# Optimization experiments

Measured on AMD Instinct MI355X. Metric: run time of the kernel, lower is better.

## Reference

```python
import jax, jax.numpy as jnp
import numpy as np

N_NODES = 100000
N_EDGES = 1600000
IN_CH, HID_CH, OUT_CH = 64, 128, 128


def setup_inputs() -> dict:
    key = jax.random.key(0)
    ks = jax.random.split(key, 10)
    x = jax.random.normal(ks[0], (N_NODES, IN_CH), dtype=jnp.float32)
    edge_index = jax.random.randint(ks[1], (2, N_EDGES), 0, N_NODES, dtype=jnp.int64 if jax.config.jax_enable_x64 else jnp.int32)
    edge_weight = jax.random.uniform(ks[2], (N_EDGES,), dtype=jnp.float32)
    def glorot(k, fan_in, fan_out):
        lim = np.sqrt(6.0 / (fan_in + fan_out)).astype(np.float32)
        return jax.random.uniform(k, (fan_in, fan_out), minval=-lim, maxval=lim, dtype=jnp.float32)
    W1 = glorot(ks[3], IN_CH, HID_CH)
    b1 = jnp.zeros((HID_CH,), jnp.float32)
    W2 = glorot(ks[4], HID_CH, HID_CH)
    b2 = jnp.zeros((HID_CH,), jnp.float32)
    W3 = glorot(ks[5], HID_CH, OUT_CH)
    b3 = jnp.zeros((OUT_CH,), jnp.float32)
    return {"x": x, "edge_index": edge_index, "edge_weight": edge_weight,
            "W1": W1, "b1": b1, "W2": W2, "b2": b2, "W3": W3, "b3": b3}


def _gcn_norm(edge_index, edge_weight, num_nodes):
    # add self-loops with weight 1 (PyG GCNConv default)
    loop = jnp.arange(num_nodes, dtype=edge_index.dtype)
    src = jnp.concatenate([edge_index[0], loop])
    dst = jnp.concatenate([edge_index[1], loop])
    w = jnp.concatenate([edge_weight, jnp.ones((num_nodes,), edge_weight.dtype)])
    deg = jax.ops.segment_sum(w, dst, num_segments=num_nodes)
    dinv = jnp.where(deg > 0, jax.lax.rsqrt(deg), 0.0)
    norm = dinv[src] * w * dinv[dst]
    return src, dst, norm


def _gcn_layer(x, W, b, src, dst, norm, num_nodes):
    h = x @ W                                  # [N, C_out]
    msg = h[src] * norm[:, None]               # gather + scale, [E+N, C_out]
    agg = jax.ops.segment_sum(msg, dst, num_segments=num_nodes)
    return agg + b


def reference(x, edge_index, edge_weight, W1, b1, W2, b2, W3, b3):
    n = x.shape[0]
    src, dst, norm = _gcn_norm(edge_index, edge_weight, n)
    h = jax.nn.silu(_gcn_layer(x, W1, b1, src, dst, norm, n))
    h = jax.nn.silu(_gcn_layer(h, W2, b2, src, dst, norm, n))
    h = jax.nn.silu(_gcn_layer(h, W3, b3, src, dst, norm, n))
    # single-graph global mean pool (batch == zeros)
    return jnp.mean(h, axis=0, keepdims=True)  # [1, out_channels]
```

## Files before the change

### kernel.cpp

```cpp
#include <hip/hip_runtime.h>

#define C 128
#define INCH 64
#define FIXP 33554432.0f

typedef unsigned short bf16_t;
typedef float f32x4 __attribute__((ext_vector_type(4)));
typedef unsigned int u32x4 __attribute__((ext_vector_type(4)));

__device__ __forceinline__ float silu_f(float v) {
    return v / (1.0f + __expf(-v));
}

__device__ __forceinline__ bf16_t f2bf(float f) {
    unsigned b = __float_as_uint(f);
    return (bf16_t)((b + 0x7FFFu + ((b >> 16) & 1u)) >> 16);
}
__device__ __forceinline__ float bf2f(unsigned u) {
    return __uint_as_float(u << 16);
}

__device__ __forceinline__ void mfma16x16x32(f32x4& d, u32x4 a, u32x4 b) {
    asm("v_mfma_f32_16x16x32_bf16 %0, %1, %2, %0" : "+v"(d) : "v"(a), "v"(b));
}


template<int NCH> struct VecN;
template<> struct VecN<4> { using T = float4; };
template<> struct VecN<2> { using T = float2; };

template<int NCH> struct LdB;
template<> struct LdB<4> {
    static __device__ __forceinline__ float4 ld(const bf16_t* p) {
        ushort4 u = *(const ushort4*)p;
        return make_float4(bf2f(u.x), bf2f(u.y), bf2f(u.z), bf2f(u.w));
    }
};
template<> struct LdB<2> {
    static __device__ __forceinline__ float2 ld(const bf16_t* p) {
        ushort2 u = *(const ushort2*)p;
        return make_float2(bf2f(u.x), bf2f(u.y));
    }
};

template<int NCH> struct StB;
template<> struct StB<4> {
    static __device__ __forceinline__ void st(bf16_t* p, float4 v) {
        *(ushort4*)p = make_ushort4(f2bf(v.x), f2bf(v.y), f2bf(v.z), f2bf(v.w));
    }
};
template<> struct StB<2> {
    static __device__ __forceinline__ void st(bf16_t* p, float2 v) {
        *(ushort2*)p = make_ushort2(f2bf(v.x), f2bf(v.y));
    }
};

__device__ __forceinline__ float4 vfma(const float4 v, float n, float4 a) {
    a.x = fmaf(v.x, n, a.x); a.y = fmaf(v.y, n, a.y);
    a.z = fmaf(v.z, n, a.z); a.w = fmaf(v.w, n, a.w); return a;
}
__device__ __forceinline__ float2 vfma(const float2 v, float n, float2 a) {
    a.x = fmaf(v.x, n, a.x); a.y = fmaf(v.y, n, a.y); return a;
}
__device__ __forceinline__ float4 vmul(const float4 v, float s) {
    return make_float4(v.x * s, v.y * s, v.z * s, v.w * s);
}
__device__ __forceinline__ float2 vmul(const float2 v, float s) {
    return make_float2(v.x * s, v.y * s);
}
__device__ __forceinline__ float4 vadd(const float4 a, const float4 b) {
    return make_float4(a.x + b.x, a.y + b.y, a.z + b.z, a.w + b.w);
}
__device__ __forceinline__ float2 vadd(const float2 a, const float2 b) {
    return make_float2(a.x + b.x, a.y + b.y);
}


__global__ void init_k(unsigned long long* packed, int n) {
    int i = blockIdx.x * blockDim.x + threadIdx.x;
    if (i < n) packed[i] = 0ull;
}

__global__ void hist_k(const int* __restrict__ dst, const float* __restrict__ w,
                       unsigned long long* packed, int* __restrict__ rank, int E) {
    int e = blockIdx.x * blockDim.x + threadIdx.x;
    if (e < E) {
        unsigned fx = (unsigned)(w[e] * FIXP + 0.5f);
        unsigned long long old =
            atomicAdd(&packed[dst[e]], (1ull << 32) | (unsigned long long)fx);
        rank[e] = (int)(old >> 32);
    }
}

__global__ void extract_k(const unsigned long long* __restrict__ packed,
                          int* counts, float* dinv, int n) {
    int i = blockIdx.x * blockDim.x + threadIdx.x;
    if (i < n) {
        unsigned long long p = packed[i];
        counts[i] = (int)(p >> 32);
        float deg = 1.0f + (float)(unsigned)(p & 0xffffffffull) * (1.0f / FIXP);
        dinv[i] = rsqrtf(deg);
    }
}


__global__ void cvt_bf16_k(const float* __restrict__ in, bf16_t* __restrict__ out, int n4) {
    int i = blockIdx.x * blockDim.x + threadIdx.x;
    if (i < n4) {
        float4 v = *(const float4*)&in[(size_t)i * 4];
        ushort4 u = make_ushort4(f2bf(v.x), f2bf(v.y), f2bf(v.z), f2bf(v.w));
        *(ushort4*)&out[(size_t)i * 4] = u;
    }
}


__global__ void wfrag_k(const float* __restrict__ W, bf16_t* __restrict__ Wf, int K) {
    int idx = blockIdx.x * blockDim.x + threadIdx.x;
    if (idx >= K * 128) return;
    int KS = K / 32;
    int j = idx & 7;
    int lane = (idx >> 3) & 63;
    int rest = idx >> 9;
    int ks = rest % KS;
    int nt = rest / KS;
    int col = nt * 16 + (lane & 15);
    int k = ks * 32 + (lane >> 4) * 8 + j;
    Wf[idx] = f2bf(W[k * 128 + col]);
}


#define SCAN_T 256
#define SCAN_E 1024

__global__ void scan1_k(const int* __restrict__ counts, int* rowptr, int* bsums, int N) {
    __shared__ int s[SCAN_T];
    int t = threadIdx.x;
    int base = blockIdx.x * SCAN_E + t * 4;
    int v[4];
    #pragma unroll
    for (int j = 0; j < 4; ++j) { int i = base + j; v[j] = (i < N) ? counts[i] : 0; }
    int sum = v[0] + v[1] + v[2] + v[3];
    s[t] = sum; __syncthreads();
    for (int off = 1; off < SCAN_T; off <<= 1) {
        int y = (t >= off) ? s[t - off] : 0;
        __syncthreads();
        s[t] += y;
        __syncthreads();
    }
    int incl = s[t];
    int excl = incl - sum;
    if (t == SCAN_T - 1) bsums[blockIdx.x] = incl;
    int run = excl;
    #pragma unroll
    for (int j = 0; j < 4; ++j) { int i = base + j; if (i < N) rowptr[i] = run; run += v[j]; }
}

__global__ void scan2_k(int* bsums, int nb) {
    __shared__ int s[128];
    int t = threadIdx.x;
    int v = (t < nb) ? bsums[t] : 0;
    s[t] = v; __syncthreads();
    for (int off = 1; off < 128; off <<= 1) {
        int y = (t >= off) ? s[t - off] : 0;
        __syncthreads();
        s[t] += y;
        __syncthreads();
    }
    if (t < nb) bsums[t] = s[t] - v;
}

__global__ void scan3_k(int* rowptr, const int* __restrict__ bsums, int N, int E) {
    int i = blockIdx.x * blockDim.x + threadIdx.x;
    if (i < N) rowptr[i] += bsums[i >> 10];
    if (i == 0) rowptr[N] = E;
}


__global__ void fill_csr_k(const int* __restrict__ src, const int* __restrict__ dst,
                           const float* __restrict__ w, const float* __restrict__ dinv,
                           const int* __restrict__ rowptr, const int* __restrict__ rank,
                           unsigned* edata, int E) {
    int e = blockIdx.x * blockDim.x + threadIdx.x;
    if (e >= E) return;
    int s = src[e], d = dst[e];
    float nm = dinv[s] * w[e] * dinv[d];
    int pos = rowptr[d] + rank[e];
    edata[pos] = ((unsigned)s << 15) | (unsigned)f2bf(nm);
}


template<int CH>
__launch_bounds__(256)
__global__ void agg_gather_k(const bf16_t* __restrict__ Xin, const unsigned* __restrict__ edata,
                             const int* __restrict__ rowptr, const float* __restrict__ dinv,
                             bf16_t* __restrict__ outbuf, int N) {
    constexpr int NCH = CH / 32;
    using VecT = typename VecN<NCH>::T;
    const int g = threadIdx.x >> 5;
    const int l = threadIdx.x & 31;
    const int d = blockIdx.x * 8 + g;
    if (d >= N) return;
    const int c = l * NCH;

    float di = dinv[d];
    float d2 = di * di;
    VecT a0 = vmul(LdB<NCH>::ld(&Xin[(size_t)d * CH + c]), d2);
    VecT a1 = {}, a2 = {}, a3 = {};
    const int beg = rowptr[d], end = rowptr[d + 1];
    for (int j = beg; j < end; j += 4) {
        int j1 = j + 1, j2 = j + 2, j3 = j + 3;
        unsigned m0 = edata[j];
        unsigned m1 = edata[j1 < end ? j1 : j];
        unsigned m2 = edata[j2 < end ? j2 : j];
        unsigned m3 = edata[j3 < end ? j3 : j];
        float n0 = bf2f(m0 & 0x7FFFu);
        float n1 = j1 < end ? bf2f(m1 & 0x7FFFu) : 0.f;
        float n2 = j2 < end ? bf2f(m2 & 0x7FFFu) : 0.f;
        float n3 = j3 < end ? bf2f(m3 & 0x7FFFu) : 0.f;
        VecT v0 = LdB<NCH>::ld(&Xin[(size_t)(m0 >> 15) * CH + c]);
        VecT v1 = LdB<NCH>::ld(&Xin[(size_t)(m1 >> 15) * CH + c]);
        VecT v2 = LdB<NCH>::ld(&Xin[(size_t)(m2 >> 15) * CH + c]);
        VecT v3 = LdB<NCH>::ld(&Xin[(size_t)(m3 >> 15) * CH + c]);
        a0 = vfma(v0, n0, a0);
        a1 = vfma(v1, n1, a1);
        a2 = vfma(v2, n2, a2);
        a3 = vfma(v3, n3, a3);
    }
    VecT acc = vadd(vadd(a0, a1), vadd(a2, a3));
    StB<NCH>::st(&outbuf[(size_t)d * CH + c], acc);
}


template<int K, bool POOL>
__launch_bounds__(256)
__global__ void gemm_mfma_k(const bf16_t* __restrict__ A, const bf16_t* __restrict__ Wf,
                            const float* __restrict__ bias, void* __restrict__ outp, int N) {
    constexpr int KS = K / 32;
    const int tid = threadIdx.x;
    const int wid = tid >> 6;
    const int lane = tid & 63;
    const int r0 = blockIdx.x * 64 + wid * 16;
    const int col = lane & 15;
    const int kgrp = lane >> 4;

    int arow = r0 + col;
    if (arow > N - 1) arow = N - 1;

    f32x4 acc[8] = {};
    #pragma unroll
    for (int ks = 0; ks < KS; ++ks) {
        u32x4 a = *(const u32x4*)(A + (size_t)arow * K + ks * 32 + kgrp * 8);
        #pragma unroll
        for (int n = 0; n < 8; ++n) {
            u32x4 b = *(const u32x4*)(Wf + ((size_t)(n * KS + ks) * 64 + lane) * 8);
            mfma16x16x32(acc[n], a, b);
        }
    }

    const int rbase = r0 + kgrp * 4;
    if (!POOL) {
        bf16_t* out = (bf16_t*)outp;
        #pragma unroll
        for (int n = 0; n < 8; ++n) {
            float bc = bias[n * 16 + col];
            #pragma unroll
            for (int j = 0; j < 4; ++j) {
                int r = rbase + j;
                if (r < N) out[(size_t)r * C + n * 16 + col] = f2bf(silu_f(acc[n][j] + bc));
            }
        }
    } else {
        float s[8];
        #pragma unroll
        for (int n = 0; n < 8; ++n) {
            float bc = bias[n * 16 + col];
            float t = 0.f;
            #pragma unroll
            for (int j = 0; j < 4; ++j) {
                int r = rbase + j;
                float v = silu_f(acc[n][j] + bc);
                t += (r < N) ? v : 0.f;
            }
            s[n] = t;
        }
        #pragma unroll
        for (int n = 0; n < 8; ++n) {
            s[n] += __shfl_xor(s[n], 16);
            s[n] += __shfl_xor(s[n], 32);
        }
        __shared__ float part[4][C];
        if (lane < 16) {
            #pragma unroll
            for (int n = 0; n < 8; ++n) part[wid][n * 16 + lane] = s[n];
        }
        __syncthreads();
        if (tid < C) {
            float t = part[0][tid] + part[1][tid] + part[2][tid] + part[3][tid];
            ((float*)outp)[(size_t)blockIdx.x * C + tid] = t;
        }
    }
}


__global__ void reduce1_k(const float* __restrict__ partial, float* __restrict__ p2,
                          int NB, int chunk) {
    int t = threadIdx.x;
    int r0 = blockIdx.x * chunk;
    int r1 = r0 + chunk; if (r1 > NB) r1 = NB;
    float s = 0.f;
    for (int r = r0; r < r1; ++r) s += partial[(size_t)r * C + t];
    p2[(size_t)blockIdx.x * C + t] = s;
}

__global__ void reduce2_k(const float* __restrict__ p2, float* __restrict__ out,
                          int R1, float inv_n) {
    int t = threadIdx.x;
    float s = 0.f;
    for (int r = 0; r < R1; ++r) s += p2[(size_t)r * C + t];
    out[t] = s * inv_n;
}


extern "C" void kernel_launch(void* const* d_in, const int* in_sizes, int n_in,
                              void* d_out, int out_size, void* d_ws, size_t ws_size,
                              hipStream_t stream) {
    const float* x  = (const float*)d_in[0];
    const int*   ei = (const int*)d_in[1];
    const float* ew = (const float*)d_in[2];
    const float* W1 = (const float*)d_in[3];
    const float* b1 = (const float*)d_in[4];
    const float* W2 = (const float*)d_in[5];
    const float* b2 = (const float*)d_in[6];
    const float* W3 = (const float*)d_in[7];
    const float* b3 = (const float*)d_in[8];
    float* out = (float*)d_out;

    const int N = in_sizes[0] / INCH;
    const int E = in_sizes[1] / 2;
    const int* src = ei;
    const int* dst = ei + E;

    char* ws = (char*)d_ws;
    size_t off = 0;
    auto alloc = [&](size_t bytes) -> void* {
        void* p = ws + off;
        off += (bytes + 255) & ~(size_t)255;
        return p;
    };
    bf16_t*   A      = (bf16_t*)  alloc((size_t)N * C * sizeof(bf16_t));
    bf16_t*   Xh     = (bf16_t*)  alloc((size_t)N * C * sizeof(bf16_t));
    bf16_t*   xh     = (bf16_t*)  alloc((size_t)N * INCH * sizeof(bf16_t));
    unsigned* edata  = (unsigned*)alloc((size_t)E * sizeof(unsigned));
    int*      rank   = (int*)     alloc((size_t)E * sizeof(int));
    int*      rowptr = (int*)     alloc((size_t)(N + 1) * sizeof(int));
    unsigned long long* packed = (unsigned long long*)alloc((size_t)N * 8);
    int*      counts = (int*)     alloc((size_t)N * sizeof(int));
    float*    dinv   = (float*)   alloc((size_t)N * sizeof(float));
    int*      bsums  = (int*)     alloc(256 * sizeof(int));
    bf16_t*   Wf1    = (bf16_t*)  alloc((size_t)INCH * C * sizeof(bf16_t));
    bf16_t*   Wf2    = (bf16_t*)  alloc((size_t)C * C * sizeof(bf16_t));
    bf16_t*   Wf3    = (bf16_t*)  alloc((size_t)C * C * sizeof(bf16_t));
    (void)ws_size;

    const int nb = (N + 255) / 256;
    const int eb = (E + 255) / 256;
    const int sbk = (N + SCAN_E - 1) / SCAN_E;

    init_k<<<nb, 256, 0, stream>>>(packed, N);
    hist_k<<<eb, 256, 0, stream>>>(dst, ew, packed, rank, E);
    extract_k<<<nb, 256, 0, stream>>>(packed, counts, dinv, N);
    scan1_k<<<sbk, SCAN_T, 0, stream>>>(counts, rowptr, bsums, N);
    scan2_k<<<1, 128, 0, stream>>>(bsums, sbk);
    scan3_k<<<nb, 256, 0, stream>>>(rowptr, bsums, N, E);
    fill_csr_k<<<eb, 256, 0, stream>>>(src, dst, ew, dinv, rowptr, rank, edata, E);
    const int cv4 = (N * INCH) / 4;
    cvt_bf16_k<<<(cv4 + 255) / 256, 256, 0, stream>>>(x, xh, cv4);
    wfrag_k<<<(INCH * C + 255) / 256, 256, 0, stream>>>(W1, Wf1, INCH);
    wfrag_k<<<(C * C + 255) / 256, 256, 0, stream>>>(W2, Wf2, C);
    wfrag_k<<<(C * C + 255) / 256, 256, 0, stream>>>(W3, Wf3, C);

    const int ab  = (N + 7) / 8;
    const int gb2 = (N + 63) / 64;

    agg_gather_k<INCH><<<ab, 256, 0, stream>>>(xh, edata, rowptr, dinv, A, N);
    gemm_mfma_k<INCH, false><<<gb2, 256, 0, stream>>>(A, Wf1, b1, Xh, N);
    agg_gather_k<C><<<ab, 256, 0, stream>>>(Xh, edata, rowptr, dinv, A, N);
    gemm_mfma_k<C, false><<<gb2, 256, 0, stream>>>(A, Wf2, b2, Xh, N);
    agg_gather_k<C><<<ab, 256, 0, stream>>>(Xh, edata, rowptr, dinv, A, N);
    float* partial = (float*)xh;
    gemm_mfma_k<C, true><<<gb2, 256, 0, stream>>>(A, Wf3, b3, partial, N);

    const int R1 = 64;
    const int chunk = (gb2 + R1 - 1) / R1;
    float* p2 = (float*)counts;
    reduce1_k<<<R1, 128, 0, stream>>>(partial, p2, gb2, chunk);
    reduce2_k<<<1, 128, 0, stream>>>(p2, out, R1, 1.0f / (float)N);
}
```

Measured before the change: 375.4 us.

## Store gathered node features in FP8 and fuse degree extraction into scan

Node features read by the neighbor-gather aggregation (the input x and the hidden activations written by the GEMM epilogue) are now stored as FP8 E4M3 instead of bf16. This halves the bytes fetched per random gather and per activation write. Decoding uses the hardware packed fp8-to-f32 conversion when it is available. The separate degree-extract kernel is folded into the first scan pass, and the zeroing kernel becomes a memset, which removes launches and one pass over node data. The trade is much lower precision on the activations that get aggregated, which raises the risk of accuracy error.

```diff
diff --git a/kernel.cpp b/kernel.cpp
--- a/kernel.cpp
+++ b/kernel.cpp
@@ -5,7 +5,9 @@
 #define FIXP 33554432.0f
 
 typedef unsigned short bf16_t;
+typedef unsigned char fp8_t;
 typedef float f32x4 __attribute__((ext_vector_type(4)));
+typedef float f32x2 __attribute__((ext_vector_type(2)));
 typedef unsigned int u32x4 __attribute__((ext_vector_type(4)));
 
 __device__ __forceinline__ float silu_f(float v) {
@@ -20,6 +22,54 @@
     return __uint_as_float(u << 16);
 }
 
+__device__ __forceinline__ fp8_t f2fp8(float f) {
+    unsigned b = __float_as_uint(f);
+    unsigned s = (b >> 24) & 0x80u;
+    unsigned a = b & 0x7FFFFFFFu;
+    if (a >= 0x43E00000u) return (fp8_t)(s | 0x7E);
+    int e = (int)(a >> 23);
+    int e8 = e - 120;
+    if (e8 <= 0) {
+        float av = __uint_as_float(a);
+        int q = (int)(av * 512.0f + 0.5f);
+        if (q > 8) q = 8;
+        return (fp8_t)(s | (unsigned)q);
+    }
+    unsigned m = a & 0x7FFFFFu;
+    unsigned m3 = m >> 20;
+    unsigned rest = m & 0xFFFFFu;
+    if (rest > 0x80000u || (rest == 0x80000u && (m3 & 1u))) m3++;
+    unsigned enc = ((unsigned)e8 << 3) + m3;
+    if (enc >= 0x7Fu) enc = 0x7Eu;
+    return (fp8_t)(s | enc);
+}
+__device__ __forceinline__ float fp82f(unsigned v) {
+    unsigned s = (v & 0x80u) << 24;
+    unsigned e = (v >> 3) & 0xFu;
+    unsigned m = v & 7u;
+    if (e) return __uint_as_float(s | ((e + 120u) << 23) | (m << 20));
+    float f = (float)m * 0.001953125f;
+    return __uint_as_float(s | __float_as_uint(f));
+}
+__device__ __forceinline__ float4 dec4(unsigned v) {
+#if __has_builtin(__builtin_amdgcn_cvt_pk_f32_fp8)
+    f32x2 lo = __builtin_amdgcn_cvt_pk_f32_fp8((int)v, false);
+    f32x2 hi = __builtin_amdgcn_cvt_pk_f32_fp8((int)v, true);
+    return make_float4(lo[0], lo[1], hi[0], hi[1]);
+#else
+    return make_float4(fp82f(v & 0xFFu), fp82f((v >> 8) & 0xFFu),
+                       fp82f((v >> 16) & 0xFFu), fp82f(v >> 24));
+#endif
+}
+__device__ __forceinline__ float2 dec2(unsigned v) {
+#if __has_builtin(__builtin_amdgcn_cvt_pk_f32_fp8)
+    f32x2 lo = __builtin_amdgcn_cvt_pk_f32_fp8((int)v, false);
+    return make_float2(lo[0], lo[1]);
+#else
+    return make_float2(fp82f(v & 0xFFu), fp82f((v >> 8) & 0xFFu));
+#endif
+}
+
 __device__ __forceinline__ void mfma16x16x32(f32x4& d, u32x4 a, u32x4 b) {
     asm("v_mfma_f32_16x16x32_bf16 %0, %1, %2, %0" : "+v"(d) : "v"(a), "v"(b));
 }
@@ -29,17 +79,15 @@
 template<> struct VecN<4> { using T = float4; };
 template<> struct VecN<2> { using T = float2; };
 
-template<int NCH> struct LdB;
-template<> struct LdB<4> {
-    static __device__ __forceinline__ float4 ld(const bf16_t* p) {
-        ushort4 u = *(const ushort4*)p;
-        return make_float4(bf2f(u.x), bf2f(u.y), bf2f(u.z), bf2f(u.w));
+template<int NCH> struct Ld8;
+template<> struct Ld8<4> {
+    static __device__ __forceinline__ float4 ld(const fp8_t* p) {
+        return dec4(*(const unsigned*)p);
     }
 };
-template<> struct LdB<2> {
-    static __device__ __forceinline__ float2 ld(const bf16_t* p) {
-        ushort2 u = *(const ushort2*)p;
-        return make_float2(bf2f(u.x), bf2f(u.y));
+template<> struct Ld8<2> {
+    static __device__ __forceinline__ float2 ld(const fp8_t* p) {
+        return dec2((unsigned)*(const unsigned short*)p);
     }
 };
 
@@ -75,11 +123,6 @@
     return make_float2(a.x + b.x, a.y + b.y);
 }
 
-
-__global__ void init_k(unsigned long long* packed, int n) {
-    int i = blockIdx.x * blockDim.x + threadIdx.x;
-    if (i < n) packed[i] = 0ull;
-}
 
 __global__ void hist_k(const int* __restrict__ dst, const float* __restrict__ w,
                        unsigned long long* packed, int* __restrict__ rank, int E) {
@@ -92,24 +135,13 @@
     }
 }
 
-__global__ void extract_k(const unsigned long long* __restrict__ packed,
-                          int* counts, float* dinv, int n) {
-    int i = blockIdx.x * blockDim.x + threadIdx.x;
-    if (i < n) {
-        unsigned long long p = packed[i];
-        counts[i] = (int)(p >> 32);
-        float deg = 1.0f + (float)(unsigned)(p & 0xffffffffull) * (1.0f / FIXP);
-        dinv[i] = rsqrtf(deg);
-    }
-}
-
-
-__global__ void cvt_bf16_k(const float* __restrict__ in, bf16_t* __restrict__ out, int n4) {
+
+__global__ void cvt_fp8_k(const float* __restrict__ in, fp8_t* __restrict__ out, int n4) {
     int i = blockIdx.x * blockDim.x + threadIdx.x;
     if (i < n4) {
         float4 v = *(const float4*)&in[(size_t)i * 4];
-        ushort4 u = make_ushort4(f2bf(v.x), f2bf(v.y), f2bf(v.z), f2bf(v.w));
-        *(ushort4*)&out[(size_t)i * 4] = u;
+        uchar4 u = make_uchar4(f2fp8(v.x), f2fp8(v.y), f2fp8(v.z), f2fp8(v.w));
+        *(uchar4*)&out[(size_t)i * 4] = u;
     }
 }
 
@@ -132,13 +164,22 @@
 #define SCAN_T 256
 #define SCAN_E 1024
 
-__global__ void scan1_k(const int* __restrict__ counts, int* rowptr, int* bsums, int N) {
+__global__ void scan1_k(const unsigned long long* __restrict__ packed,
+                        int* rowptr, int* bsums, float* __restrict__ dinv, int N) {
     __shared__ int s[SCAN_T];
     int t = threadIdx.x;
     int base = blockIdx.x * SCAN_E + t * 4;
     int v[4];
     #pragma unroll
-    for (int j = 0; j < 4; ++j) { int i = base + j; v[j] = (i < N) ? counts[i] : 0; }
+    for (int j = 0; j < 4; ++j) {
+        int i = base + j;
+        if (i < N) {
+            unsigned long long p = packed[i];
+            v[j] = (int)(p >> 32);
+            float deg = 1.0f + (float)(unsigned)(p & 0xffffffffull) * (1.0f / FIXP);
+            dinv[i] = rsqrtf(deg);
+        } else v[j] = 0;
+    }
     int sum = v[0] + v[1] + v[2] + v[3];
     s[t] = sum; __syncthreads();
     for (int off = 1; off < SCAN_T; off <<= 1) {
@@ -191,7 +232,7 @@
 
 template<int CH>
 __launch_bounds__(256)
-__global__ void agg_gather_k(const bf16_t* __restrict__ Xin, const unsigned* __restrict__ edata,
+__global__ void agg_gather_k(const fp8_t* __restrict__ Xin, const unsigned* __restrict__ edata,
                              const int* __restrict__ rowptr, const float* __restrict__ dinv,
                              bf16_t* __restrict__ outbuf, int N) {
     constexpr int NCH = CH / 32;
@@ -204,7 +245,7 @@
 
     float di = dinv[d];
     float d2 = di * di;
-    VecT a0 = vmul(LdB<NCH>::ld(&Xin[(size_t)d * CH + c]), d2);
+    VecT a0 = vmul(Ld8<NCH>::ld(&Xin[(size_t)d * CH + c]), d2);
     VecT a1 = {}, a2 = {}, a3 = {};
     const int beg = rowptr[d], end = rowptr[d + 1];
     for (int j = beg; j < end; j += 4) {
@@ -217,10 +258,10 @@
         float n1 = j1 < end ? bf2f(m1 & 0x7FFFu) : 0.f;
         float n2 = j2 < end ? bf2f(m2 & 0x7FFFu) : 0.f;
         float n3 = j3 < end ? bf2f(m3 & 0x7FFFu) : 0.f;
-        VecT v0 = LdB<NCH>::ld(&Xin[(size_t)(m0 >> 15) * CH + c]);
-        VecT v1 = LdB<NCH>::ld(&Xin[(size_t)(m1 >> 15) * CH + c]);
-        VecT v2 = LdB<NCH>::ld(&Xin[(size_t)(m2 >> 15) * CH + c]);
-        VecT v3 = LdB<NCH>::ld(&Xin[(size_t)(m3 >> 15) * CH + c]);
+        VecT v0 = Ld8<NCH>::ld(&Xin[(size_t)(m0 >> 15) * CH + c]);
+        VecT v1 = Ld8<NCH>::ld(&Xin[(size_t)(m1 >> 15) * CH + c]);
+        VecT v2 = Ld8<NCH>::ld(&Xin[(size_t)(m2 >> 15) * CH + c]);
+        VecT v3 = Ld8<NCH>::ld(&Xin[(size_t)(m3 >> 15) * CH + c]);
         a0 = vfma(v0, n0, a0);
         a1 = vfma(v1, n1, a1);
         a2 = vfma(v2, n2, a2);
@@ -259,14 +300,14 @@
 
     const int rbase = r0 + kgrp * 4;
     if (!POOL) {
-        bf16_t* out = (bf16_t*)outp;
+        fp8_t* out = (fp8_t*)outp;
         #pragma unroll
         for (int n = 0; n < 8; ++n) {
             float bc = bias[n * 16 + col];
             #pragma unroll
             for (int j = 0; j < 4; ++j) {
                 int r = rbase + j;
-                if (r < N) out[(size_t)r * C + n * 16 + col] = f2bf(silu_f(acc[n][j] + bc));
+                if (r < N) out[(size_t)r * C + n * 16 + col] = f2fp8(silu_f(acc[n][j] + bc));
             }
         }
     } else {
@@ -348,15 +389,15 @@
         return p;
     };
     bf16_t*   A      = (bf16_t*)  alloc((size_t)N * C * sizeof(bf16_t));
-    bf16_t*   Xh     = (bf16_t*)  alloc((size_t)N * C * sizeof(bf16_t));
-    bf16_t*   xh     = (bf16_t*)  alloc((size_t)N * INCH * sizeof(bf16_t));
+    fp8_t*    Xh8    = (fp8_t*)   alloc((size_t)N * C);
+    fp8_t*    x8     = (fp8_t*)   alloc((size_t)N * INCH);
     unsigned* edata  = (unsigned*)alloc((size_t)E * sizeof(unsigned));
     int*      rank   = (int*)     alloc((size_t)E * sizeof(int));
     int*      rowptr = (int*)     alloc((size_t)(N + 1) * sizeof(int));
     unsigned long long* packed = (unsigned long long*)alloc((size_t)N * 8);
-    int*      counts = (int*)     alloc((size_t)N * sizeof(int));
     float*    dinv   = (float*)   alloc((size_t)N * sizeof(float));
     int*      bsums  = (int*)     alloc(256 * sizeof(int));
+    float*    p2     = (float*)   alloc(64 * C * sizeof(float));
     bf16_t*   Wf1    = (bf16_t*)  alloc((size_t)INCH * C * sizeof(bf16_t));
     bf16_t*   Wf2    = (bf16_t*)  alloc((size_t)C * C * sizeof(bf16_t));
     bf16_t*   Wf3    = (bf16_t*)  alloc((size_t)C * C * sizeof(bf16_t));
@@ -366,15 +407,14 @@
     const int eb = (E + 255) / 256;
     const int sbk = (N + SCAN_E - 1) / SCAN_E;
 
-    init_k<<<nb, 256, 0, stream>>>(packed, N);
+    hipMemsetAsync(packed, 0, (size_t)N * 8, stream);
     hist_k<<<eb, 256, 0, stream>>>(dst, ew, packed, rank, E);
-    extract_k<<<nb, 256, 0, stream>>>(packed, counts, dinv, N);
-    scan1_k<<<sbk, SCAN_T, 0, stream>>>(counts, rowptr, bsums, N);
+    scan1_k<<<sbk, SCAN_T, 0, stream>>>(packed, rowptr, bsums, dinv, N);
     scan2_k<<<1, 128, 0, stream>>>(bsums, sbk);
     scan3_k<<<nb, 256, 0, stream>>>(rowptr, bsums, N, E);
     fill_csr_k<<<eb, 256, 0, stream>>>(src, dst, ew, dinv, rowptr, rank, edata, E);
     const int cv4 = (N * INCH) / 4;
-    cvt_bf16_k<<<(cv4 + 255) / 256, 256, 0, stream>>>(x, xh, cv4);
+    cvt_fp8_k<<<(cv4 + 255) / 256, 256, 0, stream>>>(x, x8, cv4);
     wfrag_k<<<(INCH * C + 255) / 256, 256, 0, stream>>>(W1, Wf1, INCH);
     wfrag_k<<<(C * C + 255) / 256, 256, 0, stream>>>(W2, Wf2, C);
     wfrag_k<<<(C * C + 255) / 256, 256, 0, stream>>>(W3, Wf3, C);
@@ -382,17 +422,16 @@
     const int ab  = (N + 7) / 8;
     const int gb2 = (N + 63) / 64;
 
-    agg_gather_k<INCH><<<ab, 256, 0, stream>>>(xh, edata, rowptr, dinv, A, N);
-    gemm_mfma_k<INCH, false><<<gb2, 256, 0, stream>>>(A, Wf1, b1, Xh, N);
-    agg_gather_k<C><<<ab, 256, 0, stream>>>(Xh, edata, rowptr, dinv, A, N);
-    gemm_mfma_k<C, false><<<gb2, 256, 0, stream>>>(A, Wf2, b2, Xh, N);
-    agg_gather_k<C><<<ab, 256, 0, stream>>>(Xh, edata, rowptr, dinv, A, N);
-    float* partial = (float*)xh;
+    agg_gather_k<INCH><<<ab, 256, 0, stream>>>(x8, edata, rowptr, dinv, A, N);
+    gemm_mfma_k<INCH, false><<<gb2, 256, 0, stream>>>(A, Wf1, b1, Xh8, N);
+    agg_gather_k<C><<<ab, 256, 0, stream>>>(Xh8, edata, rowptr, dinv, A, N);
+    gemm_mfma_k<C, false><<<gb2, 256, 0, stream>>>(A, Wf2, b2, Xh8, N);
+    agg_gather_k<C><<<ab, 256, 0, stream>>>(Xh8, edata, rowptr, dinv, A, N);
+    float* partial = (float*)x8;
     gemm_mfma_k<C, true><<<gb2, 256, 0, stream>>>(A, Wf3, b3, partial, N);
 
     const int R1 = 64;
     const int chunk = (gb2 + R1 - 1) / R1;
-    float* p2 = (float*)counts;
     reduce1_k<<<R1, 128, 0, stream>>>(partial, p2, gb2, chunk);
     reduce2_k<<<1, 128, 0, stream>>>(p2, out, R1, 1.0f / (float)N);
 }
```

Result: faster. 338.6 us (-9.8%).
